# Kernel optimization log

Hardware: AMD Instinct MI355X
Metric: run time of the kernel (lower is better)

The kernel has to match this reference:

```python
import jax, jax.numpy as jnp
import numpy as np

B, T, C, HS = 4, 4096, 1024, 128

def setup_inputs() -> dict:
    key = jax.random.key(0)
    kx, kq, kk, kv = jax.random.split(key, 4)
    x = jax.random.normal(kx, (B, T, C), dtype=jnp.float32)
    # bias-free Linear weights, stored as (in, out) so projection is x @ W
    scale = 1.0 / np.sqrt(C)
    Wq = jax.random.normal(kq, (C, HS), dtype=jnp.float32) * scale
    Wk = jax.random.normal(kk, (C, HS), dtype=jnp.float32) * scale
    Wv = jax.random.normal(kv, (C, HS), dtype=jnp.float32) * scale
    return {"x": x, "Wq": Wq, "Wk": Wk, "Wv": Wv}

def reference(x, Wq, Wk, Wv):
    # x: (B,T,C) -> q,k,v: (B,T,HS)
    q = jnp.einsum('btc,ch->bth', x, Wq)
    k = jnp.einsum('btc,ch->bth', x, Wk)
    v = jnp.einsum('btc,ch->bth', x, Wv)
    hs = k.shape[-1]
    # scaled scores (B,T,T) with causal mask
    wei = jnp.einsum('bth,bsh->bts', q, k) * (hs ** -0.5)
    causal = jnp.tril(jnp.ones((q.shape[1], q.shape[1]), dtype=bool))
    wei = jnp.where(causal, wei, -jnp.inf)
    wei = jax.nn.softmax(wei, axis=-1)
    # dropout p=0.0 -> identity
    out = jnp.einsum('bts,bsh->bth', wei, v)
    return out
```

## Files before the change

### kernel.cpp

```cpp
#include <hip/hip_runtime.h>
#include <hip/hip_bf16.h>

typedef __attribute__((ext_vector_type(8))) short short8;
typedef __attribute__((ext_vector_type(4))) float f32x4;

#define BATCH 4
#define TLEN 4096
#define CDIM 1024
#define HSD 128
#define MROWS (BATCH*TLEN)

__device__ __forceinline__ unsigned short f2bf(float f){
    unsigned u = __builtin_bit_cast(unsigned, f);
    u = (u + 0x7FFFu + ((u >> 16) & 1u)) >> 16;
    return (unsigned short)u;
}

__global__ void prep_w_k(const float* __restrict__ Wq, const float* __restrict__ Wk,
                         const float* __restrict__ Wv, unsigned short* __restrict__ Wt){
    int idx = blockIdx.x * 256 + threadIdx.x;
    const int total = 3 * HSD * CDIM;
    if (idx >= total) return;
    int w = idx / (HSD * CDIM);
    int r = idx - w * HSD * CDIM;
    int h = r / CDIM;
    int c = r - h * CDIM;
    const float* W = (w == 0) ? Wq : ((w == 1) ? Wk : Wv);
    Wt[idx] = f2bf(W[c * HSD + h]);
}

__global__ void prep_x_k(const float* __restrict__ x, unsigned short* __restrict__ xb){
    int i = (blockIdx.x * 256 + threadIdx.x) * 8;
    float4 a = *(const float4*)(x + i);
    float4 b = *(const float4*)(x + i + 4);
    short8 o;
    o[0]=(short)f2bf(a.x); o[1]=(short)f2bf(a.y); o[2]=(short)f2bf(a.z); o[3]=(short)f2bf(a.w);
    o[4]=(short)f2bf(b.x); o[5]=(short)f2bf(b.y); o[6]=(short)f2bf(b.z); o[7]=(short)f2bf(b.w);
    *(short8*)(xb + i) = o;
}

__device__ __forceinline__ void stage_tile32(unsigned short* buf, const unsigned short* g,
                                             int ldg, int tid){
#pragma unroll
    for (int i = 0; i < 2; i++){
        int c = i * 256 + tid;
        int row = c >> 2, kp = c & 3;
        int swz = (row & 3) ^ ((row >> 2) & 3);
        const unsigned short* gp = g + (size_t)row * ldg + ((kp ^ swz) << 3);
        unsigned short* lp = buf + (c << 3);
        __builtin_amdgcn_global_load_lds((const __attribute__((address_space(1))) void*)gp,
                                         (__attribute__((address_space(3))) void*)lp, 16, 0, 0);
    }
}

__global__ __launch_bounds__(256) void proj_k(const unsigned short* __restrict__ xb,
                                              const unsigned short* __restrict__ Wt,
                                              unsigned short* __restrict__ Qb,
                                              unsigned short* __restrict__ Kb,
                                              unsigned short* __restrict__ Vt){
    __shared__ unsigned short As[2][128 * 32];
    __shared__ unsigned short Bs[2][128 * 32];

    const int tid = threadIdx.x, lane = tid & 63, wave = tid >> 6;
    const int m = lane & 15, quad = lane >> 4;
    const int wr = wave & 1, wc = wave >> 1;
    const int rb = blockIdx.x * 128;
    const int p  = blockIdx.y;

    const unsigned short* gA = xb + (size_t)rb * CDIM;
    const unsigned short* gB = Wt + (size_t)(p * HSD) * CDIM;

    f32x4 acc[4][4];
#pragma unroll
    for (int i = 0; i < 4; i++)
#pragma unroll
        for (int j = 0; j < 4; j++) acc[i][j] = (f32x4)0.f;

    stage_tile32(&As[0][0], gA, CDIM, tid);
    stage_tile32(&Bs[0][0], gB, CDIM, tid);
    __syncthreads();

    int cur = 0;
    for (int kc = 0; kc < CDIM / 32; ++kc){
        if (kc + 1 < CDIM / 32){
            stage_tile32(&As[cur ^ 1][0], gA + (kc + 1) * 32, CDIM, tid);
            stage_tile32(&Bs[cur ^ 1][0], gB + (kc + 1) * 32, CDIM, tid);
        }
        const unsigned short* Af = (p == 2) ? &As[cur][0] : &Bs[cur][0];
        const unsigned short* Bf = (p == 2) ? &Bs[cur][0] : &As[cur][0];
        short8 aF[4], bF[4];
#pragma unroll
        for (int i = 0; i < 4; i++){
            int ra = wr * 64 + i * 16 + m;
            int sa = (ra & 3) ^ ((ra >> 2) & 3);
            aF[i] = *(const short8*)&Af[ra * 32 + ((quad ^ sa) << 3)];
            int rn = wc * 64 + i * 16 + m;
            int sb = (rn & 3) ^ ((rn >> 2) & 3);
            bF[i] = *(const short8*)&Bf[rn * 32 + ((quad ^ sb) << 3)];
        }
#pragma unroll
        for (int i = 0; i < 4; i++)
#pragma unroll
            for (int j = 0; j < 4; j++)
                acc[i][j] = __builtin_amdgcn_mfma_f32_16x16x32_bf16(aF[i], bF[j], acc[i][j], 0, 0, 0);
        __syncthreads();
        cur ^= 1;
    }

    if (p < 2){
        unsigned short* D = (p == 0) ? Qb : Kb;
#pragma unroll
        for (int i = 0; i < 4; i++){
#pragma unroll
            for (int j = 0; j < 4; j++){
                int h = wr * 64 + i * 16 + quad * 4;
                int t = rb + wc * 64 + j * 16 + m;
                ushort4 v;
                v.x = f2bf(acc[i][j][0]); v.y = f2bf(acc[i][j][1]);
                v.z = f2bf(acc[i][j][2]); v.w = f2bf(acc[i][j][3]);
                *(ushort4*)(D + (size_t)t * HSD + h) = v;
            }
        }
    } else {
        int b = rb >> 12;
        int tb = rb & 4095;
#pragma unroll
        for (int i = 0; i < 4; i++){
#pragma unroll
            for (int j = 0; j < 4; j++){
                int t = tb + wr * 64 + i * 16 + quad * 4;
                int h = wc * 64 + j * 16 + m;
                ushort4 v;
                v.x = f2bf(acc[i][j][0]); v.y = f2bf(acc[i][j][1]);
                v.z = f2bf(acc[i][j][2]); v.w = f2bf(acc[i][j][3]);
                *(ushort4*)(Vt + ((size_t)b * HSD + h) * TLEN + t) = v;
            }
        }
    }
}

__global__ void proj_f32_k(const float* __restrict__ x, const unsigned short* __restrict__ Wt,
                           unsigned short* __restrict__ Qb, unsigned short* __restrict__ Kb,
                           unsigned short* __restrict__ Vt){
    const int lane = threadIdx.x;
    const int m = lane & 15, quad = lane >> 4;
    const int rb = blockIdx.x * 16;

    f32x4 acc[3][8];
#pragma unroll
    for (int p = 0; p < 3; p++)
#pragma unroll
        for (int i = 0; i < 8; i++) acc[p][i] = (f32x4)0.f;

    const float* xrow = x + (size_t)(rb + m) * CDIM + quad * 8;
    for (int k0 = 0; k0 < CDIM; k0 += 32){
        float4 a0 = *(const float4*)(xrow + k0);
        float4 a1 = *(const float4*)(xrow + k0 + 4);
        short8 aF;
        aF[0]=(short)f2bf(a0.x); aF[1]=(short)f2bf(a0.y); aF[2]=(short)f2bf(a0.z); aF[3]=(short)f2bf(a0.w);
        aF[4]=(short)f2bf(a1.x); aF[5]=(short)f2bf(a1.y); aF[6]=(short)f2bf(a1.z); aF[7]=(short)f2bf(a1.w);
#pragma unroll
        for (int p = 0; p < 3; p++){
#pragma unroll
            for (int sub = 0; sub < 8; sub++){
                short8 bF = *(const short8*)(Wt + (size_t)(p * HSD + sub * 16 + m) * CDIM + k0 + quad * 8);
                acc[p][sub] = __builtin_amdgcn_mfma_f32_16x16x32_bf16(aF, bF, acc[p][sub], 0, 0, 0);
            }
        }
    }
#pragma unroll
    for (int p = 0; p < 3; p++){
#pragma unroll
        for (int sub = 0; sub < 8; sub++){
#pragma unroll
            for (int r = 0; r < 4; r++){
                int row = rb + quad * 4 + r;
                int col = sub * 16 + m;
                unsigned short v = f2bf(acc[p][sub][r]);
                if (p == 0)      Qb[(size_t)row * HSD + col] = v;
                else if (p == 1) Kb[(size_t)row * HSD + col] = v;
                else {
                    int b = row >> 12;
                    int t = row & 4095;
                    Vt[((size_t)b * HSD + col) * TLEN + t] = v;
                }
            }
        }
    }
}

__device__ __forceinline__ void stage_k_tile(unsigned short* buf, const unsigned short* g,
                                             int wave, int lane){
#pragma unroll
    for (int i = 0; i < 4; i++){
        int slot = wave * 256 + i * 64 + lane;
        int row = slot >> 4;
        int ch  = slot & 15;
        const unsigned short* gp = g + row * 128 + ((ch ^ (row & 15)) << 3);
        unsigned short* lp = buf + ((wave * 256 + i * 64) << 3);
        __builtin_amdgcn_global_load_lds((const __attribute__((address_space(1))) void*)gp,
                                         (__attribute__((address_space(3))) void*)lp, 16, 0, 0);
    }
}
__device__ __forceinline__ void stage_v_tile(unsigned short* buf, const unsigned short* g,
                                             int wave, int lane){
#pragma unroll
    for (int i = 0; i < 4; i++){
        int slot = wave * 256 + i * 64 + lane;
        int row = slot >> 3;
        int ch  = slot & 7;
        const unsigned short* gp = g + (size_t)row * TLEN + ((ch ^ (row & 7)) << 3);
        unsigned short* lp = buf + ((wave * 256 + i * 64) << 3);
        __builtin_amdgcn_global_load_lds((const __attribute__((address_space(1))) void*)gp,
                                         (__attribute__((address_space(3))) void*)lp, 16, 0, 0);
    }
}

__global__ __launch_bounds__(256) void attn_k(const unsigned short* __restrict__ Qb,
                       const unsigned short* __restrict__ Kb,
                       const unsigned short* __restrict__ Vts,
                       float* __restrict__ Opart, float2* __restrict__ ml, int seglen){
    __shared__ unsigned short Kt[2][64 * 128];
    __shared__ unsigned short Vs[2][128 * 64];
    __shared__ unsigned short Pl[4][16 * 72];

    const int tid = threadIdx.x, lane = tid & 63, wave = tid >> 6;
    const int m = lane & 15, quad = lane >> 4;
    const int q0 = blockIdx.x * 64;
    const int seg = blockIdx.y, b = blockIdx.z;
    const int g0 = seg * seglen;
    if (g0 >= q0 + 64) return;
    const int gend = min(g0 + seglen, q0 + 64);
    const int nT = (gend - g0) >> 6;
    const float scale = 0.08838834764831845f;

    const size_t rowg = (size_t)b * TLEN + q0 + wave * 16;

    short8 aQ[4];
#pragma unroll
    for (int kk = 0; kk < 4; kk++)
        aQ[kk] = *(const short8*)(Qb + (rowg + m) * HSD + kk * 32 + quad * 8);

    f32x4 accO[8];
#pragma unroll
    for (int i = 0; i < 8; i++) accO[i] = (f32x4)0.f;
    float mi[4], li[4];
#pragma unroll
    for (int r = 0; r < 4; r++){ mi[r] = -1e30f; li[r] = 0.f; }

    const unsigned short* kbase = Kb + (size_t)b * TLEN * HSD;
    const unsigned short* vbase = Vts + (size_t)b * HSD * TLEN;

    stage_k_tile(&Kt[0][0], kbase + (size_t)g0 * HSD, wave, lane);
    stage_v_tile(&Vs[0][0], vbase + g0, wave, lane);
    __syncthreads();

    int cur = 0;
    for (int t = 0; t < nT; ++t){
        const int s0 = g0 + t * 64;
        if (t + 1 < nT){
            stage_k_tile(&Kt[cur ^ 1][0], kbase + (size_t)(s0 + 64) * HSD, wave, lane);
            stage_v_tile(&Vs[cur ^ 1][0], vbase + (s0 + 64), wave, lane);
        }
        f32x4 S[4];
#pragma unroll
        for (int ns = 0; ns < 4; ns++){
            f32x4 sa = (f32x4)0.f;
#pragma unroll
            for (int kk = 0; kk < 4; kk++){
                short8 bK = *(const short8*)&Kt[cur][(ns * 16 + m) * 128 + (((kk * 4 + quad) ^ m) << 3)];
                sa = __builtin_amdgcn_mfma_f32_16x16x32_bf16(aQ[kk], bK, sa, 0, 0, 0);
            }
#pragma unroll
            for (int r = 0; r < 4; r++) sa[r] *= scale;
            S[ns] = sa;
        }
        if (s0 + 63 > q0 + wave * 16){
#pragma unroll
            for (int ns = 0; ns < 4; ns++){
                int sg = s0 + ns * 16 + m;
#pragma unroll
                for (int r = 0; r < 4; r++){
                    int qrow = q0 + wave * 16 + quad * 4 + r;
                    if (sg > qrow) S[ns][r] = -1e30f;
                }
            }
        }
        float mloc[4];
#pragma unroll
        for (int r = 0; r < 4; r++)
            mloc[r] = fmaxf(fmaxf(S[0][r], S[1][r]), fmaxf(S[2][r], S[3][r]));
#pragma unroll
        for (int off = 1; off < 16; off <<= 1)
#pragma unroll
            for (int r = 0; r < 4; r++)
                mloc[r] = fmaxf(mloc[r], __shfl_xor(mloc[r], off, 64));
        float al[4];
#pragma unroll
        for (int r = 0; r < 4; r++){
            float mn = fmaxf(mi[r], mloc[r]);
            al[r] = __expf(mi[r] - mn);
            mi[r] = mn;
        }
        float lsum[4] = {0.f, 0.f, 0.f, 0.f};
#pragma unroll
        for (int ns = 0; ns < 4; ns++){
#pragma unroll
            for (int r = 0; r < 4; r++){
                float pv = __expf(S[ns][r] - mi[r]);
                lsum[r] += pv;
                Pl[wave][(quad * 4 + r) * 72 + ns * 16 + m] = f2bf(pv);
            }
        }
#pragma unroll
        for (int off = 1; off < 16; off <<= 1)
#pragma unroll
            for (int r = 0; r < 4; r++)
                lsum[r] += __shfl_xor(lsum[r], off, 64);
#pragma unroll
        for (int r = 0; r < 4; r++) li[r] = li[r] * al[r] + lsum[r];
#pragma unroll
        for (int sub = 0; sub < 8; sub++)
#pragma unroll
            for (int r = 0; r < 4; r++) accO[sub][r] *= al[r];
        short8 aP[2];
#pragma unroll
        for (int t2 = 0; t2 < 2; t2++)
            aP[t2] = *(const short8*)&Pl[wave][m * 72 + t2 * 32 + quad * 8];
#pragma unroll
        for (int sub = 0; sub < 8; sub++){
#pragma unroll
            for (int t2 = 0; t2 < 2; t2++){
                short8 bV = *(const short8*)&Vs[cur][(sub * 16 + m) * 64 + (((t2 * 4 + quad) ^ (m & 7)) << 3)];
                accO[sub] = __builtin_amdgcn_mfma_f32_16x16x32_bf16(aP[t2], bV, accO[sub], 0, 0, 0);
            }
        }
        __syncthreads();
        cur ^= 1;
    }
    if (m == 0){
#pragma unroll
        for (int r = 0; r < 4; r++){
            float2 v; v.x = mi[r]; v.y = li[r];
            ml[(size_t)seg * MROWS + rowg + quad * 4 + r] = v;
        }
    }
    float* ob = Opart + (size_t)seg * MROWS * HSD;
#pragma unroll
    for (int sub = 0; sub < 8; sub++)
#pragma unroll
        for (int r = 0; r < 4; r++)
            ob[(rowg + quad * 4 + r) * HSD + sub * 16 + m] = accO[sub][r];
}

__global__ void merge_k(const float* __restrict__ Opart, const float2* __restrict__ ml,
                        float* __restrict__ out, int nseg, int seglen){
    int idx = blockIdx.x * 256 + threadIdx.x;
    int row = idx >> 7;
    int t = row & (TLEN - 1);
    int q0 = t & ~63;
    int nsv = min(nseg, (q0 + 63) / seglen + 1);
    float M = -1e30f;
    for (int s = 0; s < nsv; s++) M = fmaxf(M, ml[(size_t)s * MROWS + row].x);
    float L = 0.f, o = 0.f;
    for (int s = 0; s < nsv; s++){
        float2 p = ml[(size_t)s * MROWS + row];
        float w = __expf(p.x - M);
        L += p.y * w;
        o += w * Opart[(size_t)s * MROWS * HSD + idx];
    }
    out[idx] = o / L;
}

extern "C" void kernel_launch(void* const* d_in, const int* in_sizes, int n_in,
                              void* d_out, int out_size, void* d_ws, size_t ws_size,
                              hipStream_t stream) {
    const float* x  = (const float*)d_in[0];
    const float* Wq = (const float*)d_in[1];
    const float* Wk = (const float*)d_in[2];
    const float* Wv = (const float*)d_in[3];
    float* out = (float*)d_out;
    char* w = (char*)d_ws;

    unsigned short* Wt = (unsigned short*)w;
    unsigned short *xb = nullptr, *Qb, *Kb, *Vt;
    float* Opart; float2* ml;
    int nseg; bool use_xb;

    if (ws_size >= (size_t)78u * 1024 * 1024){
        nseg = 4; use_xb = true;
        xb = (unsigned short*)(w + ((size_t)1u  << 20));
        Qb = (unsigned short*)(w + ((size_t)33u << 20));
        Kb = (unsigned short*)(w + ((size_t)37u << 20));
        Vt = (unsigned short*)(w + ((size_t)41u << 20));
        Opart = (float*)(w + ((size_t)45u << 20));
        ml    = (float2*)(w + ((size_t)77u << 20));
    } else if (ws_size >= (size_t)46u * 1024 * 1024){
        nseg = 1; use_xb = true;
        xb = (unsigned short*)(w + ((size_t)1u  << 20));
        Qb = (unsigned short*)(w + ((size_t)33u << 20));
        Kb = (unsigned short*)(w + ((size_t)37u << 20));
        Vt = (unsigned short*)(w + ((size_t)41u << 20));
        Opart = out;
        ml    = (float2*)(w + ((size_t)45u << 20));
    } else {
        nseg = 1; use_xb = false;
        Qb = (unsigned short*)(w + ((size_t)1u << 20));
        Kb = (unsigned short*)(w + ((size_t)5u << 20));
        Vt = (unsigned short*)(w + ((size_t)9u << 20));
        Opart = out;
        ml    = (float2*)(w + ((size_t)13u << 20));
    }
    const int seglen = TLEN / nseg;

    prep_w_k<<<(3 * HSD * CDIM + 255) / 256, 256, 0, stream>>>(Wq, Wk, Wv, Wt);
    if (use_xb){
        prep_x_k<<<(MROWS * CDIM) / (256 * 8), 256, 0, stream>>>(x, xb);
        proj_k<<<dim3(MROWS / 128, 3), 256, 0, stream>>>(xb, Wt, Qb, Kb, Vt);
    } else {
        proj_f32_k<<<MROWS / 16, 64, 0, stream>>>(x, Wt, Qb, Kb, Vt);
    }
    attn_k<<<dim3(TLEN / 64, nseg, BATCH), 256, 0, stream>>>(Qb, Kb, Vt, Opart, ml, seglen);
    merge_k<<<(MROWS * HSD) / 256, 256, 0, stream>>>(Opart, ml, out, nseg, seglen);
}
```

Baseline: 220.8 us.

## Compute transposed scores in registers, fold scale into Q, drop LDS P roundtrip

Folds the softmax scale and log2(e) into Q at projection time so the attention kernel can use exp2 directly. It computes S transposed (K as the A operand) so each lane owns one query row, which shrinks the row max and sum reductions to two shuffles. P is packed to bf16 in registers and fed to 16x16x16 MFMAs, removing the per-wave LDS staging of P. The K/V double buffer is replaced by a single buffer with launch_bounds(256,4) to raise occupancy, and query blocks are scheduled heaviest-first. The cost is that global-to-LDS loads no longer overlap with compute, and the alpha rescale needs a ds_bpermute.

```diff
diff --git a/kernel.cpp b/kernel.cpp
--- a/kernel.cpp
+++ b/kernel.cpp
@@ -2,6 +2,7 @@
 #include <hip/hip_bf16.h>
 
 typedef __attribute__((ext_vector_type(8))) short short8;
+typedef __attribute__((ext_vector_type(4))) short s4v;
 typedef __attribute__((ext_vector_type(4))) float f32x4;
 
 #define BATCH 4
@@ -10,10 +11,23 @@
 #define HSD 128
 #define MROWS (BATCH*TLEN)
 
+#define QSCALE 0.12751744f
+
+#ifdef __HIP_DEVICE_COMPILE__
+  #define MFMA16(a,b,c) __builtin_amdgcn_mfma_f32_16x16x16bf16_1k(a,b,c,0,0,0)
+#else
+  #define MFMA16(a,b,c) (c)
+#endif
+
 __device__ __forceinline__ unsigned short f2bf(float f){
     unsigned u = __builtin_bit_cast(unsigned, f);
     u = (u + 0x7FFFu + ((u >> 16) & 1u)) >> 16;
     return (unsigned short)u;
+}
+__device__ __forceinline__ unsigned pkbf(float a, float b){
+    unsigned ua = (__builtin_bit_cast(unsigned, a) + 0x8000u) >> 16;
+    unsigned ub = (__builtin_bit_cast(unsigned, b) + 0x8000u) & 0xFFFF0000u;
+    return ua | ub;
 }
 
 __global__ void prep_w_k(const float* __restrict__ Wq, const float* __restrict__ Wk,
@@ -109,6 +123,7 @@
 
     if (p < 2){
         unsigned short* D = (p == 0) ? Qb : Kb;
+        const float qs = (p == 0) ? QSCALE : 1.0f;
 #pragma unroll
         for (int i = 0; i < 4; i++){
 #pragma unroll
@@ -116,8 +131,8 @@
                 int h = wr * 64 + i * 16 + quad * 4;
                 int t = rb + wc * 64 + j * 16 + m;
                 ushort4 v;
-                v.x = f2bf(acc[i][j][0]); v.y = f2bf(acc[i][j][1]);
-                v.z = f2bf(acc[i][j][2]); v.w = f2bf(acc[i][j][3]);
+                v.x = f2bf(acc[i][j][0] * qs); v.y = f2bf(acc[i][j][1] * qs);
+                v.z = f2bf(acc[i][j][2] * qs); v.w = f2bf(acc[i][j][3] * qs);
                 *(ushort4*)(D + (size_t)t * HSD + h) = v;
             }
         }
@@ -170,13 +185,14 @@
     }
 #pragma unroll
     for (int p = 0; p < 3; p++){
+        const float qs = (p == 0) ? QSCALE : 1.0f;
 #pragma unroll
         for (int sub = 0; sub < 8; sub++){
 #pragma unroll
             for (int r = 0; r < 4; r++){
                 int row = rb + quad * 4 + r;
                 int col = sub * 16 + m;
-                unsigned short v = f2bf(acc[p][sub][r]);
+                unsigned short v = f2bf(acc[p][sub][r] * qs);
                 if (p == 0)      Qb[(size_t)row * HSD + col] = v;
                 else if (p == 1) Kb[(size_t)row * HSD + col] = v;
                 else {
@@ -197,7 +213,7 @@
         int row = slot >> 4;
         int ch  = slot & 15;
         const unsigned short* gp = g + row * 128 + ((ch ^ (row & 15)) << 3);
-        unsigned short* lp = buf + ((wave * 256 + i * 64) << 3);
+        unsigned short* lp = buf + (slot << 3);
         __builtin_amdgcn_global_load_lds((const __attribute__((address_space(1))) void*)gp,
                                          (__attribute__((address_space(3))) void*)lp, 16, 0, 0);
     }
@@ -210,31 +226,30 @@
         int row = slot >> 3;
         int ch  = slot & 7;
         const unsigned short* gp = g + (size_t)row * TLEN + ((ch ^ (row & 7)) << 3);
-        unsigned short* lp = buf + ((wave * 256 + i * 64) << 3);
+        unsigned short* lp = buf + (slot << 3);
         __builtin_amdgcn_global_load_lds((const __attribute__((address_space(1))) void*)gp,
                                          (__attribute__((address_space(3))) void*)lp, 16, 0, 0);
     }
 }
 
-__global__ __launch_bounds__(256) void attn_k(const unsigned short* __restrict__ Qb,
+__global__ __launch_bounds__(256, 4) void attn_k(const unsigned short* __restrict__ Qb,
                        const unsigned short* __restrict__ Kb,
                        const unsigned short* __restrict__ Vts,
                        float* __restrict__ Opart, float2* __restrict__ ml, int seglen){
-    __shared__ unsigned short Kt[2][64 * 128];
-    __shared__ unsigned short Vs[2][128 * 64];
-    __shared__ unsigned short Pl[4][16 * 72];
+    __shared__ unsigned short Kt[64 * 128];
+    __shared__ unsigned short Vs[128 * 64];
 
     const int tid = threadIdx.x, lane = tid & 63, wave = tid >> 6;
     const int m = lane & 15, quad = lane >> 4;
-    const int q0 = blockIdx.x * 64;
+    const int q0 = ((int)gridDim.x - 1 - (int)blockIdx.x) * 64;
     const int seg = blockIdx.y, b = blockIdx.z;
     const int g0 = seg * seglen;
     if (g0 >= q0 + 64) return;
     const int gend = min(g0 + seglen, q0 + 64);
     const int nT = (gend - g0) >> 6;
-    const float scale = 0.08838834764831845f;
-
-    const size_t rowg = (size_t)b * TLEN + q0 + wave * 16;
+
+    const int q0w = q0 + wave * 16;
+    const size_t rowg = (size_t)b * TLEN + q0w;
 
     short8 aQ[4];
 #pragma unroll
@@ -244,106 +259,97 @@
     f32x4 accO[8];
 #pragma unroll
     for (int i = 0; i < 8; i++) accO[i] = (f32x4)0.f;
-    float mi[4], li[4];
-#pragma unroll
-    for (int r = 0; r < 4; r++){ mi[r] = -1e30f; li[r] = 0.f; }
+    float mi = -1e30f, li = 0.f;
 
     const unsigned short* kbase = Kb + (size_t)b * TLEN * HSD;
     const unsigned short* vbase = Vts + (size_t)b * HSD * TLEN;
-
-    stage_k_tile(&Kt[0][0], kbase + (size_t)g0 * HSD, wave, lane);
-    stage_v_tile(&Vs[0][0], vbase + g0, wave, lane);
-    __syncthreads();
-
-    int cur = 0;
+    const int bpbase = (lane >> 4) << 4;
+
     for (int t = 0; t < nT; ++t){
         const int s0 = g0 + t * 64;
-        if (t + 1 < nT){
-            stage_k_tile(&Kt[cur ^ 1][0], kbase + (size_t)(s0 + 64) * HSD, wave, lane);
-            stage_v_tile(&Vs[cur ^ 1][0], vbase + (s0 + 64), wave, lane);
-        }
+        stage_k_tile(&Kt[0], kbase + (size_t)s0 * HSD, wave, lane);
+        stage_v_tile(&Vs[0], vbase + s0, wave, lane);
+        __syncthreads();
+
         f32x4 S[4];
 #pragma unroll
         for (int ns = 0; ns < 4; ns++){
             f32x4 sa = (f32x4)0.f;
 #pragma unroll
             for (int kk = 0; kk < 4; kk++){
-                short8 bK = *(const short8*)&Kt[cur][(ns * 16 + m) * 128 + (((kk * 4 + quad) ^ m) << 3)];
-                sa = __builtin_amdgcn_mfma_f32_16x16x32_bf16(aQ[kk], bK, sa, 0, 0, 0);
-            }
-#pragma unroll
-            for (int r = 0; r < 4; r++) sa[r] *= scale;
+                short8 bK = *(const short8*)&Kt[(ns * 16 + m) * 128 + (((kk * 4 + quad) ^ m) << 3)];
+                sa = __builtin_amdgcn_mfma_f32_16x16x32_bf16(bK, aQ[kk], sa, 0, 0, 0);
+            }
             S[ns] = sa;
         }
-        if (s0 + 63 > q0 + wave * 16){
+        if (s0 + 63 > q0w){
+            int qg = q0w + m;
 #pragma unroll
             for (int ns = 0; ns < 4; ns++){
-                int sg = s0 + ns * 16 + m;
 #pragma unroll
                 for (int r = 0; r < 4; r++){
-                    int qrow = q0 + wave * 16 + quad * 4 + r;
-                    if (sg > qrow) S[ns][r] = -1e30f;
+                    int sg = s0 + ns * 16 + quad * 4 + r;
+                    if (sg > qg) S[ns][r] = -1e30f;
                 }
             }
         }
-        float mloc[4];
+        f32x4 m4 = S[0];
+#pragma unroll
+        for (int ns = 1; ns < 4; ns++)
+#pragma unroll
+            for (int r = 0; r < 4; r++) m4[r] = fmaxf(m4[r], S[ns][r]);
+        float mloc = fmaxf(fmaxf(m4[0], m4[1]), fmaxf(m4[2], m4[3]));
+        mloc = fmaxf(mloc, __shfl_xor(mloc, 16, 64));
+        mloc = fmaxf(mloc, __shfl_xor(mloc, 32, 64));
+        float mn = fmaxf(mi, mloc);
+        float al = exp2f(mi - mn);
+        mi = mn;
+
+        float ps[4][4];
+        float lsum = 0.f;
+#pragma unroll
+        for (int ns = 0; ns < 4; ns++)
+#pragma unroll
+            for (int r = 0; r < 4; r++){
+                float pv = exp2f(S[ns][r] - mi);
+                ps[ns][r] = pv;
+                lsum += pv;
+            }
+        lsum += __shfl_xor(lsum, 16, 64);
+        lsum += __shfl_xor(lsum, 32, 64);
+        li = li * al + lsum;
+
+        s4v aP[4];
+#pragma unroll
+        for (int ns = 0; ns < 4; ns++){
+            uint2 u;
+            u.x = pkbf(ps[ns][0], ps[ns][1]);
+            u.y = pkbf(ps[ns][2], ps[ns][3]);
+            aP[ns] = __builtin_bit_cast(s4v, u);
+        }
+        float alr[4];
 #pragma unroll
         for (int r = 0; r < 4; r++)
-            mloc[r] = fmaxf(fmaxf(S[0][r], S[1][r]), fmaxf(S[2][r], S[3][r]));
-#pragma unroll
-        for (int off = 1; off < 16; off <<= 1)
-#pragma unroll
-            for (int r = 0; r < 4; r++)
-                mloc[r] = fmaxf(mloc[r], __shfl_xor(mloc[r], off, 64));
-        float al[4];
-#pragma unroll
-        for (int r = 0; r < 4; r++){
-            float mn = fmaxf(mi[r], mloc[r]);
-            al[r] = __expf(mi[r] - mn);
-            mi[r] = mn;
-        }
-        float lsum[4] = {0.f, 0.f, 0.f, 0.f};
-#pragma unroll
-        for (int ns = 0; ns < 4; ns++){
-#pragma unroll
-            for (int r = 0; r < 4; r++){
-                float pv = __expf(S[ns][r] - mi[r]);
-                lsum[r] += pv;
-                Pl[wave][(quad * 4 + r) * 72 + ns * 16 + m] = f2bf(pv);
-            }
-        }
-#pragma unroll
-        for (int off = 1; off < 16; off <<= 1)
-#pragma unroll
-            for (int r = 0; r < 4; r++)
-                lsum[r] += __shfl_xor(lsum[r], off, 64);
-#pragma unroll
-        for (int r = 0; r < 4; r++) li[r] = li[r] * al[r] + lsum[r];
+            alr[r] = __builtin_bit_cast(float,
+                __builtin_amdgcn_ds_bpermute(bpbase + 4 * r, __builtin_bit_cast(int, al)));
 #pragma unroll
         for (int sub = 0; sub < 8; sub++)
 #pragma unroll
-            for (int r = 0; r < 4; r++) accO[sub][r] *= al[r];
-        short8 aP[2];
-#pragma unroll
-        for (int t2 = 0; t2 < 2; t2++)
-            aP[t2] = *(const short8*)&Pl[wave][m * 72 + t2 * 32 + quad * 8];
+            for (int r = 0; r < 4; r++) accO[sub][r] *= alr[r];
 #pragma unroll
         for (int sub = 0; sub < 8; sub++){
 #pragma unroll
-            for (int t2 = 0; t2 < 2; t2++){
-                short8 bV = *(const short8*)&Vs[cur][(sub * 16 + m) * 64 + (((t2 * 4 + quad) ^ (m & 7)) << 3)];
-                accO[sub] = __builtin_amdgcn_mfma_f32_16x16x32_bf16(aP[t2], bV, accO[sub], 0, 0, 0);
+            for (int ns = 0; ns < 4; ns++){
+                s4v bV = *(const s4v*)&Vs[(sub * 16 + m) * 64 +
+                        (((2 * ns + (quad >> 1)) ^ (m & 7)) << 3) + (quad & 1) * 4];
+                accO[sub] = MFMA16(aP[ns], bV, accO[sub]);
             }
         }
         __syncthreads();
-        cur ^= 1;
-    }
-    if (m == 0){
-#pragma unroll
-        for (int r = 0; r < 4; r++){
-            float2 v; v.x = mi[r]; v.y = li[r];
-            ml[(size_t)seg * MROWS + rowg + quad * 4 + r] = v;
-        }
+    }
+    if (quad == 0){
+        float2 v; v.x = mi; v.y = li;
+        ml[(size_t)seg * MROWS + rowg + m] = v;
     }
     float* ob = Opart + (size_t)seg * MROWS * HSD;
 #pragma unroll
@@ -365,7 +371,7 @@
     float L = 0.f, o = 0.f;
     for (int s = 0; s < nsv; s++){
         float2 p = ml[(size_t)s * MROWS + row];
-        float w = __expf(p.x - M);
+        float w = exp2f(p.x - M);
         L += p.y * w;
         o += w * Opart[(size_t)s * MROWS * HSD + idx];
     }
```

Result: faster. 214.1 us (-3.1%).
